# Performance work log

Hardware: AMD Instinct MI355X
Metric: run time of the kernel (lower is better)

Reference implementation:

```python
import jax, jax.numpy as jnp
import numpy as np

MARGIN = 0.2  # init margin
B, D = 4096, 512


def _pairwise_dist(x):
    # torch.cdist(x, x, p=2): Euclidean distance via Gram matrix
    sq = jnp.sum(x * x, axis=-1)                      # [B]
    gram = x @ x.T                                    # [B, B]
    d2 = jnp.maximum(sq[:, None] + sq[None, :] - 2.0 * gram, 0.0)
    safe = jnp.where(d2 > 0, d2, 1.0)                 # grad-safe sqrt at 0
    return jnp.where(d2 > 0, jnp.sqrt(safe), 0.0)


def setup_inputs() -> dict:
    key = jax.random.key(0)
    k1, k2, k3 = jax.random.split(key, 3)
    anchor = jax.random.normal(k1, (B, D), dtype=jnp.float32)
    positive = jax.random.normal(k2, (B, D), dtype=jnp.float32)
    labels = jax.random.randint(k3, (B,), 0, 64)
    return {"anchor": anchor, "positive": positive, "labels": labels}


def reference(anchor, positive, labels):
    d_ap = jnp.sum((anchor - positive) ** 2, axis=-1)          # [B] squared dist
    pd = _pairwise_dist(anchor)                                 # [B, B] euclidean
    diff_label = labels[None, :] != labels[:, None]             # [B, B]
    inf = jnp.float32(jnp.inf)
    # negatives farther than the positive (note: pd is euclidean, d_ap squared,
    # exactly as in the original code)
    cand = jnp.where(diff_label & (pd > d_ap[:, None]), pd, inf)
    min_larger = jnp.min(cand, axis=1)
    # fallback: min over all different-label negatives
    fallback = jnp.min(jnp.where(diff_label, pd, inf), axis=1)
    d_an = jnp.where(jnp.isfinite(min_larger), min_larger, fallback)
    loss = jnp.maximum(d_ap - d_an + MARGIN, 0.0)
    return jnp.mean(loss)
```

## Files before the change

kernel.cpp:

```cpp
#include <hip/hip_runtime.h>
#include <hip/hip_bf16.h>
#include <cstdint>
#include <cstddef>

constexpr int BN = 4096;
constexpr int DN = 512;
constexpr float MARGIN = 0.2f;
constexpr uint32_t INF_U = 0x7f800000u;

typedef __attribute__((ext_vector_type(8))) short short8;
typedef __attribute__((ext_vector_type(4))) float float4v;

#define AS1(p) ((const __attribute__((address_space(1))) void*)(p))
#define AS3(p) ((__attribute__((address_space(3))) void*)(p))

__global__ __launch_bounds__(256) void prep_kernel(
    const float* __restrict__ anchor,
    const float* __restrict__ positive,
    uint16_t* __restrict__ Abf,
    float* __restrict__ sqn,
    float* __restrict__ dap,
    uint32_t* __restrict__ min_all,
    uint32_t* __restrict__ min_larger)
{
    const int tid  = threadIdx.x;
    const int wave = tid >> 6;
    const int lane = tid & 63;
    const int row  = blockIdx.x * 4 + wave;

    const float4* arow = (const float4*)(anchor   + (size_t)row * DN);
    const float4* prow = (const float4*)(positive + (size_t)row * DN);

    float4 av0 = arow[lane * 2 + 0], av1 = arow[lane * 2 + 1];
    float4 pv0 = prow[lane * 2 + 0], pv1 = prow[lane * 2 + 1];

    float a[8] = {av0.x, av0.y, av0.z, av0.w, av1.x, av1.y, av1.z, av1.w};
    float p[8] = {pv0.x, pv0.y, pv0.z, pv0.w, pv1.x, pv1.y, pv1.z, pv1.w};

    float s = 0.f, d = 0.f;
    union { uint16_t u[8]; uint4 v; } pk;
    #pragma unroll
    for (int i = 0; i < 8; ++i) {
        s += a[i] * a[i];
        float dx = a[i] - p[i];
        d += dx * dx;
        uint32_t ub = __float_as_uint(a[i]);
        pk.u[i] = (uint16_t)((ub + 0x7fffu + ((ub >> 16) & 1u)) >> 16);
    }

    ((uint4*)(Abf + (size_t)row * DN))[lane] = pk.v;

    #pragma unroll
    for (int off = 32; off; off >>= 1) {
        s += __shfl_xor(s, off);
        d += __shfl_xor(d, off);
    }
    if (lane == 0) {
        sqn[row] = s;
        dap[row] = d;
        min_all[row]    = INF_U;
        min_larger[row] = INF_U;
    }
}

__global__ __launch_bounds__(256) void gram_kernel(
    const uint16_t* __restrict__ Abf,
    const float* __restrict__ sqn,
    const float* __restrict__ dap,
    const int* __restrict__ labels,
    uint32_t* __restrict__ min_all,
    uint32_t* __restrict__ min_larger)
{
    __shared__ uint16_t Abuf[128 * 32];
    __shared__ uint16_t Bbuf[128 * 32];

    const int tid  = threadIdx.x;
    const int wave = tid >> 6;
    const int lane = tid & 63;
    const int wi   = wave >> 1;
    const int wj   = wave & 1;
    const int quad = lane >> 4;
    const int l15  = lane & 15;

    const int rowBase = blockIdx.x * 128;
    const int colBase = blockIdx.y * 128;

    float4v acc[4][4];
    #pragma unroll
    for (int i = 0; i < 4; ++i)
        #pragma unroll
        for (int j = 0; j < 4; ++j)
            acc[i][j] = (float4v){0.f, 0.f, 0.f, 0.f};

    const int ldRow   = lane >> 2;
    const int ldChunk = lane & 3;

    for (int kt = 0; kt < DN / 32; ++kt) {
        const int k0 = kt * 32;
        __syncthreads();
        #pragma unroll
        for (int p = 0; p < 2; ++p) {
            const int r = p * 64 + wave * 16;
            const uint16_t* ga = Abf + (size_t)(rowBase + r + ldRow) * DN + k0 + ldChunk * 8;
            __builtin_amdgcn_global_load_lds(AS1(ga), AS3(Abuf + r * 32), 16, 0, 0);
            const uint16_t* gb = Abf + (size_t)(colBase + r + ldRow) * DN + k0 + ldChunk * 8;
            __builtin_amdgcn_global_load_lds(AS1(gb), AS3(Bbuf + r * 32), 16, 0, 0);
        }
        __syncthreads();

        short8 a_frag[4], b_frag[4];
        #pragma unroll
        for (int mi = 0; mi < 4; ++mi)
            a_frag[mi] = *(const short8*)(Abuf + (wi * 64 + mi * 16 + l15) * 32 + quad * 8);
        #pragma unroll
        for (int mj = 0; mj < 4; ++mj)
            b_frag[mj] = *(const short8*)(Bbuf + (wj * 64 + mj * 16 + l15) * 32 + quad * 8);

        #pragma unroll
        for (int mi = 0; mi < 4; ++mi)
            #pragma unroll
            for (int mj = 0; mj < 4; ++mj)
                acc[mi][mj] = __builtin_amdgcn_mfma_f32_16x16x32_bf16(
                    a_frag[mi], b_frag[mj], acc[mi][mj], 0, 0, 0);
    }

    const float INFF = __uint_as_float(INF_U);
    float sqj[4]; int labj[4];
    #pragma unroll
    for (int mj = 0; mj < 4; ++mj) {
        int col = colBase + wj * 64 + mj * 16 + l15;
        sqj[mj]  = sqn[col];
        labj[mj] = labels[col];
    }
    #pragma unroll
    for (int mi = 0; mi < 4; ++mi) {
        #pragma unroll
        for (int r = 0; r < 4; ++r) {
            int row = rowBase + wi * 64 + mi * 16 + quad * 4 + r;
            float sqi  = sqn[row];
            int   li   = labels[row];
            float dapi = dap[row];
            float mAll = INFF, mLarger = INFF;
            #pragma unroll
            for (int mj = 0; mj < 4; ++mj) {
                float g  = acc[mi][mj][r];
                float d2 = sqi + sqj[mj] - 2.0f * g;
                float pd = d2 > 0.f ? sqrtf(d2) : 0.f;
                if (labj[mj] != li) {
                    mAll = fminf(mAll, pd);
                    if (pd > dapi) mLarger = fminf(mLarger, pd);
                }
            }
            #pragma unroll
            for (int off = 1; off < 16; off <<= 1) {
                mAll    = fminf(mAll,    __shfl_xor(mAll, off));
                mLarger = fminf(mLarger, __shfl_xor(mLarger, off));
            }
            if (l15 == 0) {
                atomicMin(&min_all[row],    __float_as_uint(mAll));
                atomicMin(&min_larger[row], __float_as_uint(mLarger));
            }
        }
    }
}

__global__ __launch_bounds__(256) void finalize_kernel(
    const float* __restrict__ dap,
    const uint32_t* __restrict__ min_all,
    const uint32_t* __restrict__ min_larger,
    float* __restrict__ out)
{
    const int tid = threadIdx.x;
    float s = 0.f;
    for (int i = tid; i < BN; i += 256) {
        uint32_t mlu = min_larger[i];
        float dan = (mlu != INF_U) ? __uint_as_float(mlu) : __uint_as_float(min_all[i]);
        float l = dap[i] - dan + MARGIN;
        s += l > 0.f ? l : 0.f;
    }
    #pragma unroll
    for (int off = 32; off; off >>= 1) s += __shfl_xor(s, off);
    __shared__ float wsum[4];
    if ((tid & 63) == 0) wsum[tid >> 6] = s;
    __syncthreads();
    if (tid == 0) out[0] = (wsum[0] + wsum[1] + wsum[2] + wsum[3]) * (1.0f / BN);
}

extern "C" void kernel_launch(void* const* d_in, const int* in_sizes, int n_in,
                              void* d_out, int out_size, void* d_ws, size_t ws_size,
                              hipStream_t stream) {
    const float* anchor   = (const float*)d_in[0];
    const float* positive = (const float*)d_in[1];
    const int*   labels   = (const int*)d_in[2];
    float* out = (float*)d_out;

    uint8_t* ws = (uint8_t*)d_ws;
    uint16_t* Abf       = (uint16_t*)ws;
    float*    sqn       = (float*)(ws + (size_t)BN * DN * 2);
    float*    dap       = sqn + BN;
    uint32_t* min_all   = (uint32_t*)(dap + BN);
    uint32_t* min_larger = min_all + BN;

    prep_kernel<<<BN / 4, 256, 0, stream>>>(anchor, positive, Abf, sqn, dap, min_all, min_larger);
    gram_kernel<<<dim3(BN / 128, BN / 128), 256, 0, stream>>>(Abf, sqn, dap, labels, min_all, min_larger);
    finalize_kernel<<<1, 256, 0, stream>>>(dap, min_all, min_larger, out);
}
```

Before: 127.9 us.

## Exploit Gram matrix symmetry, compare squared distances, and register-prefetch swizzled tiles

Launches only upper-triangular 128x128 tiles and, for off-diagonal tiles, also reduces column-wise minima so each pair is computed once. Per-element sqrt is removed by comparing squared distances against squared d_ap, with the sqrt deferred to the finalize kernel. Global-to-LDS loads are replaced with register prefetch of the next 64-wide K tile into an XOR-swizzled LDS layout. This adds extra column reductions and atomics per tile and more register pressure in exchange for roughly half the MFMA and load work.

```diff
diff --git a/kernel.cpp b/kernel.cpp
--- a/kernel.cpp
+++ b/kernel.cpp
@@ -5,14 +5,12 @@
 
 constexpr int BN = 4096;
 constexpr int DN = 512;
+constexpr int NT = BN / 128;
 constexpr float MARGIN = 0.2f;
 constexpr uint32_t INF_U = 0x7f800000u;
 
 typedef __attribute__((ext_vector_type(8))) short short8;
 typedef __attribute__((ext_vector_type(4))) float float4v;
-
-#define AS1(p) ((const __attribute__((address_space(1))) void*)(p))
-#define AS3(p) ((__attribute__((address_space(3))) void*)(p))
 
 __global__ __launch_bounds__(256) void prep_kernel(
     const float* __restrict__ anchor,
@@ -71,8 +69,15 @@
     uint32_t* __restrict__ min_all,
     uint32_t* __restrict__ min_larger)
 {
-    __shared__ uint16_t Abuf[128 * 32];
-    __shared__ uint16_t Bbuf[128 * 32];
+    __shared__ uint16_t Abuf[128 * 64];
+    __shared__ uint16_t Bbuf[128 * 64];
+
+    int t = blockIdx.x, bi = 0, rem = NT;
+    while (t >= rem) { t -= rem; ++bi; --rem; }
+    const int bj = bi + t;
+    const bool offdiag = (bi != bj);
+    const int rowBase = bi * 128;
+    const int colBase = bj * 128;
 
     const int tid  = threadIdx.x;
     const int wave = tid >> 6;
@@ -82,8 +87,22 @@
     const int quad = lane >> 4;
     const int l15  = lane & 15;
 
-    const int rowBase = blockIdx.x * 128;
-    const int colBase = blockIdx.y * 128;
+    int sr[4], sc[4], sp[4];
+    #pragma unroll
+    for (int i = 0; i < 4; ++i) {
+        int l = tid + i * 256;
+        sr[i] = l >> 3; sc[i] = l & 7; sp[i] = sc[i] ^ (sr[i] & 7);
+    }
+
+    uint4 aS[4], bS[4];
+    auto prefetch = [&](int k0) {
+        #pragma unroll
+        for (int i = 0; i < 4; ++i) {
+            aS[i] = *(const uint4*)(Abf + (size_t)(rowBase + sr[i]) * DN + k0 + sc[i] * 8);
+            bS[i] = *(const uint4*)(Abf + (size_t)(colBase + sr[i]) * DN + k0 + sc[i] * 8);
+        }
+    };
+    prefetch(0);
 
     float4v acc[4][4];
     #pragma unroll
@@ -92,46 +111,54 @@
         for (int j = 0; j < 4; ++j)
             acc[i][j] = (float4v){0.f, 0.f, 0.f, 0.f};
 
-    const int ldRow   = lane >> 2;
-    const int ldChunk = lane & 3;
-
-    for (int kt = 0; kt < DN / 32; ++kt) {
-        const int k0 = kt * 32;
+    for (int kt = 0; kt < DN / 64; ++kt) {
         __syncthreads();
         #pragma unroll
-        for (int p = 0; p < 2; ++p) {
-            const int r = p * 64 + wave * 16;
-            const uint16_t* ga = Abf + (size_t)(rowBase + r + ldRow) * DN + k0 + ldChunk * 8;
-            __builtin_amdgcn_global_load_lds(AS1(ga), AS3(Abuf + r * 32), 16, 0, 0);
-            const uint16_t* gb = Abf + (size_t)(colBase + r + ldRow) * DN + k0 + ldChunk * 8;
-            __builtin_amdgcn_global_load_lds(AS1(gb), AS3(Bbuf + r * 32), 16, 0, 0);
+        for (int i = 0; i < 4; ++i) {
+            *(uint4*)(Abuf + sr[i] * 64 + sp[i] * 8) = aS[i];
+            *(uint4*)(Bbuf + sr[i] * 64 + sp[i] * 8) = bS[i];
         }
         __syncthreads();
-
-        short8 a_frag[4], b_frag[4];
-        #pragma unroll
-        for (int mi = 0; mi < 4; ++mi)
-            a_frag[mi] = *(const short8*)(Abuf + (wi * 64 + mi * 16 + l15) * 32 + quad * 8);
-        #pragma unroll
-        for (int mj = 0; mj < 4; ++mj)
-            b_frag[mj] = *(const short8*)(Bbuf + (wj * 64 + mj * 16 + l15) * 32 + quad * 8);
-
-        #pragma unroll
-        for (int mi = 0; mi < 4; ++mi)
-            #pragma unroll
-            for (int mj = 0; mj < 4; ++mj)
-                acc[mi][mj] = __builtin_amdgcn_mfma_f32_16x16x32_bf16(
-                    a_frag[mi], b_frag[mj], acc[mi][mj], 0, 0, 0);
+        if (kt < DN / 64 - 1) prefetch((kt + 1) * 64);
+
+        #pragma unroll
+        for (int kk = 0; kk < 2; ++kk) {
+            short8 af[4], bfr[4];
+            #pragma unroll
+            for (int mi = 0; mi < 4; ++mi) {
+                int r = wi * 64 + mi * 16 + l15;
+                int p = (kk * 4 + quad) ^ (r & 7);
+                af[mi] = *(const short8*)(Abuf + r * 64 + p * 8);
+            }
+            #pragma unroll
+            for (int mj = 0; mj < 4; ++mj) {
+                int r = wj * 64 + mj * 16 + l15;
+                int p = (kk * 4 + quad) ^ (r & 7);
+                bfr[mj] = *(const short8*)(Bbuf + r * 64 + p * 8);
+            }
+            #pragma unroll
+            for (int mi = 0; mi < 4; ++mi)
+                #pragma unroll
+                for (int mj = 0; mj < 4; ++mj)
+                    acc[mi][mj] = __builtin_amdgcn_mfma_f32_16x16x32_bf16(
+                        af[mi], bfr[mj], acc[mi][mj], 0, 0, 0);
+        }
     }
 
     const float INFF = __uint_as_float(INF_U);
-    float sqj[4]; int labj[4];
+    float sqj[4], dapj2[4]; int labj[4];
     #pragma unroll
     for (int mj = 0; mj < 4; ++mj) {
         int col = colBase + wj * 64 + mj * 16 + l15;
         sqj[mj]  = sqn[col];
         labj[mj] = labels[col];
-    }
+        float dj = dap[col];
+        dapj2[mj] = dj * dj;
+    }
+    float cAll[4], cLarger[4];
+    #pragma unroll
+    for (int mj = 0; mj < 4; ++mj) { cAll[mj] = INFF; cLarger[mj] = INFF; }
+
     #pragma unroll
     for (int mi = 0; mi < 4; ++mi) {
         #pragma unroll
@@ -140,15 +167,19 @@
             float sqi  = sqn[row];
             int   li   = labels[row];
             float dapi = dap[row];
+            float dapi2 = dapi * dapi;
             float mAll = INFF, mLarger = INFF;
             #pragma unroll
             for (int mj = 0; mj < 4; ++mj) {
-                float g  = acc[mi][mj][r];
-                float d2 = sqi + sqj[mj] - 2.0f * g;
-                float pd = d2 > 0.f ? sqrtf(d2) : 0.f;
+                float d2 = sqi + sqj[mj] - 2.0f * acc[mi][mj][r];
+                d2 = d2 > 0.f ? d2 : 0.f;
                 if (labj[mj] != li) {
-                    mAll = fminf(mAll, pd);
-                    if (pd > dapi) mLarger = fminf(mLarger, pd);
+                    mAll = fminf(mAll, d2);
+                    if (d2 > dapi2) mLarger = fminf(mLarger, d2);
+                    if (offdiag) {
+                        cAll[mj] = fminf(cAll[mj], d2);
+                        if (d2 > dapj2[mj]) cLarger[mj] = fminf(cLarger[mj], d2);
+                    }
                 }
             }
             #pragma unroll
@@ -159,6 +190,19 @@
             if (l15 == 0) {
                 atomicMin(&min_all[row],    __float_as_uint(mAll));
                 atomicMin(&min_larger[row], __float_as_uint(mLarger));
+            }
+        }
+    }
+    if (offdiag) {
+        #pragma unroll
+        for (int mj = 0; mj < 4; ++mj) {
+            float a0 = cAll[mj], l0 = cLarger[mj];
+            a0 = fminf(a0, __shfl_xor(a0, 16)); l0 = fminf(l0, __shfl_xor(l0, 16));
+            a0 = fminf(a0, __shfl_xor(a0, 32)); l0 = fminf(l0, __shfl_xor(l0, 32));
+            if (quad == 0) {
+                int col = colBase + wj * 64 + mj * 16 + l15;
+                atomicMin(&min_all[col],    __float_as_uint(a0));
+                atomicMin(&min_larger[col], __float_as_uint(l0));
             }
         }
     }
@@ -174,7 +218,8 @@
     float s = 0.f;
     for (int i = tid; i < BN; i += 256) {
         uint32_t mlu = min_larger[i];
-        float dan = (mlu != INF_U) ? __uint_as_float(mlu) : __uint_as_float(min_all[i]);
+        float dan2 = (mlu != INF_U) ? __uint_as_float(mlu) : __uint_as_float(min_all[i]);
+        float dan = sqrtf(dan2);
         float l = dap[i] - dan + MARGIN;
         s += l > 0.f ? l : 0.f;
     }
@@ -195,13 +240,13 @@
     float* out = (float*)d_out;
 
     uint8_t* ws = (uint8_t*)d_ws;
-    uint16_t* Abf       = (uint16_t*)ws;
-    float*    sqn       = (float*)(ws + (size_t)BN * DN * 2);
-    float*    dap       = sqn + BN;
-    uint32_t* min_all   = (uint32_t*)(dap + BN);
+    uint16_t* Abf        = (uint16_t*)ws;
+    float*    sqn        = (float*)(ws + (size_t)BN * DN * 2);
+    float*    dap        = sqn + BN;
+    uint32_t* min_all    = (uint32_t*)(dap + BN);
     uint32_t* min_larger = min_all + BN;
 
     prep_kernel<<<BN / 4, 256, 0, stream>>>(anchor, positive, Abf, sqn, dap, min_all, min_larger);
-    gram_kernel<<<dim3(BN / 128, BN / 128), 256, 0, stream>>>(Abf, sqn, dap, labels, min_all, min_larger);
+    gram_kernel<<<NT * (NT + 1) / 2, 256, 0, stream>>>(Abf, sqn, dap, labels, min_all, min_larger);
     finalize_kernel<<<1, 256, 0, stream>>>(dap, min_all, min_larger, out);
 }
```

After: 154.5 us. +20.8%, slower.
